# Optimization experiments

Measured on AMD Instinct MI355X. Metric: run time of the kernel, lower is better.

Reference implementation:

```python
import jax, jax.numpy as jnp
import numpy as np

N_NODES = 100000
N_EDGES = 1600000
NFEAT, NHID, NCLASS = 128, 64, 16


def setup_inputs() -> dict:
    key = jax.random.key(0)
    k1, k2, k3, k4, k5 = jax.random.split(key, 5)
    x = jax.random.normal(k1, (N_NODES, NFEAT), dtype=jnp.float32)
    edge_index = jax.random.randint(k2, (2, N_EDGES), 0, N_NODES, dtype=jnp.int64)
    edge_weight = jax.random.uniform(k3, (N_EDGES,), dtype=jnp.float32)
    # PyG Linear default init ~ kaiming-uniform; plain scaled normals suffice as a baseline
    W1 = jax.random.normal(k4, (NFEAT, NHID), dtype=jnp.float32) / np.sqrt(NFEAT)
    W2 = jax.random.normal(k5, (NHID, NCLASS), dtype=jnp.float32) / np.sqrt(NHID)
    return {"x": x, "edge_index": edge_index, "edge_weight": edge_weight, "W1": W1, "W2": W2}


def _gcn_conv(x, W, src, dst, w, num_nodes):
    # GCNConv(normalize=False, add_self_loops=False, bias=False):
    # out[dst] = sum_{e: dst(e)=dst} w_e * (x @ W)[src(e)]
    h = x @ W                                    # [N, out]
    msg = w[:, None] * h[src]                    # [E, out] gathered messages
    return jax.ops.segment_sum(msg, dst, num_segments=num_nodes)


def reference(x, edge_index, edge_weight, W1, W2):
    src, dst = edge_index[0], edge_index[1]
    h = jax.nn.relu(_gcn_conv(x, W1, src, dst, edge_weight, N_NODES))
    out = _gcn_conv(h, W2, src, dst, edge_weight, N_NODES)
    return out
```

## Files before the change

### kernel.cpp

```cpp
#include <hip/hip_runtime.h>

#define N_NODES 100000
#define N_EDGES 1600000
#define NFEAT 128
#define NHID 64
#define NCLASS 16

#define NPB 196
#define NB 511
#define HIST_EPT 16
#define HIST_BLOCKS ((N_EDGES + 256 * HIST_EPT - 1) / (256 * HIST_EPT))
#define FILL_EPT 8
#define FILL_BLOCKS ((N_EDGES + 256 * FILL_EPT - 1) / (256 * FILL_EPT))
#define NTILES ((N_NODES + 15) / 16)
#define GEMM_BLOCKS ((NTILES + 3) / 4)

typedef unsigned int u32;
typedef __attribute__((ext_vector_type(8))) short bf16x8;
typedef __attribute__((ext_vector_type(4))) float f32x4;

__device__ __forceinline__ u32 pack_bf16(float a, float b) {
    u32 ua = __float_as_uint(a);
    u32 ub = __float_as_uint(b);
    ua = (ua + 0x7fffu + ((ua >> 16) & 1u)) >> 16;
    ub = (ub + 0x7fffu + ((ub >> 16) & 1u)) >> 16;
    return ua | (ub << 16);
}
__device__ __forceinline__ short f2bf(float f) {
    u32 u = __float_as_uint(f);
    u = (u + 0x7fffu + ((u >> 16) & 1u)) >> 16;
    return (short)u;
}
__device__ __forceinline__ float bf16_lo(u32 u) { return __uint_as_float(u << 16); }
__device__ __forceinline__ float bf16_hi(u32 u) { return __uint_as_float(u & 0xffff0000u); }

__global__ void detect_kernel(const u32* __restrict__ ei, int* __restrict__ flag) {
    __shared__ int any_nz;
    if (threadIdx.x == 0) any_nz = 0;
    __syncthreads();
    u32 v = ei[2 * threadIdx.x + 1];
    if (v != 0) any_nz = 1;
    __syncthreads();
    if (threadIdx.x == 0) *flag = any_nz;
}

__device__ __forceinline__ int load_idx(const void* ei, int flag, size_t pos) {
    return flag ? ((const int*)ei)[pos] : (int)((const long long*)ei)[pos];
}

__global__ __launch_bounds__(256) void histA_kernel(const void* __restrict__ ei,
                                                    const int* __restrict__ flag,
                                                    int* __restrict__ ghist) {
    __shared__ int cnt[512];
    int t = threadIdx.x;
    cnt[t] = 0;
    cnt[t + 256] = 0;
    __syncthreads();
    int f = *flag;
    int base = blockIdx.x * 256 * HIST_EPT;
#pragma unroll
    for (int k = 0; k < HIST_EPT; ++k) {
        int e = base + k * 256 + t;
        if (e < N_EDGES) {
            int d = load_idx(ei, f, (size_t)N_EDGES + e);
            atomicAdd(&cnt[d / NPB], 1);
        }
    }
    __syncthreads();
    if (cnt[t] > 0) atomicAdd(&ghist[t], cnt[t]);
    if (cnt[t + 256] > 0) atomicAdd(&ghist[t + 256], cnt[t + 256]);
}

__global__ __launch_bounds__(512) void scanA_kernel(const int* __restrict__ ghist,
                                                    int* __restrict__ bstart,
                                                    int* __restrict__ gcursor) {
    __shared__ int lds[512];
    int t = threadIdx.x;
    int own = (t < NB) ? ghist[t] : 0;
    lds[t] = own;
    __syncthreads();
    for (int off = 1; off < 512; off <<= 1) {
        int v = (t >= off) ? lds[t - off] : 0;
        __syncthreads();
        lds[t] += v;
        __syncthreads();
    }
    int excl = lds[t] - own;
    bstart[t] = excl;
    if (t == 511) bstart[512] = lds[511];
    if (t < NB) gcursor[t] = excl;
}

__global__ __launch_bounds__(256) void fillA_kernel(const void* __restrict__ ei,
                                                    const int* __restrict__ flag,
                                                    const float* __restrict__ ew,
                                                    int* __restrict__ gcursor,
                                                    int2* __restrict__ ebuf) {
    __shared__ int cnt[512];
    __shared__ int base[512];
    int t = threadIdx.x;
    cnt[t] = 0;
    cnt[t + 256] = 0;
    __syncthreads();
    int f = *flag;
    int eb = blockIdx.x * 256 * FILL_EPT;
    int src[FILL_EPT], bin[FILL_EPT], rank[FILL_EPT];
    float w[FILL_EPT];
#pragma unroll
    for (int k = 0; k < FILL_EPT; ++k) {
        int e = eb + k * 256 + t;
        bin[k] = -1;
        if (e < N_EDGES) {
            int s = load_idx(ei, f, (size_t)e);
            int d = load_idx(ei, f, (size_t)N_EDGES + e);
            int b = d / NPB;
            src[k] = s | ((d - b * NPB) << 20);
            w[k] = ew[e];
            bin[k] = b;
            rank[k] = atomicAdd(&cnt[b], 1);
        }
    }
    __syncthreads();
    if (cnt[t] > 0) base[t] = atomicAdd(&gcursor[t], cnt[t]);
    if (cnt[t + 256] > 0) base[t + 256] = atomicAdd(&gcursor[t + 256], cnt[t + 256]);
    __syncthreads();
#pragma unroll
    for (int k = 0; k < FILL_EPT; ++k) {
        if (bin[k] >= 0) {
            int pos = base[bin[k]] + rank[k];
            ebuf[pos] = make_int2(src[k], __float_as_int(w[k]));
        }
    }
}

__global__ __launch_bounds__(256) void sortB_kernel(const int2* __restrict__ ebuf,
                                                    const int* __restrict__ bstart,
                                                    int2* __restrict__ ebuf2,
                                                    int* __restrict__ row_ptr) {
    __shared__ int cnt[NPB];
    __shared__ int sc[256];
    __shared__ int cur[NPB];
    int t = threadIdx.x, b = blockIdx.x;
    for (int i = t; i < NPB; i += 256) cnt[i] = 0;
    __syncthreads();
    int start = bstart[b], end = bstart[b + 1];
    for (int i = start + t; i < end; i += 256) {
        int dl = ((u32)ebuf[i].x) >> 20;
        atomicAdd(&cnt[dl], 1);
    }
    __syncthreads();
    int own = (t < NPB) ? cnt[t] : 0;
    sc[t] = own;
    __syncthreads();
    for (int off = 1; off < 256; off <<= 1) {
        int v = (t >= off) ? sc[t - off] : 0;
        __syncthreads();
        sc[t] += v;
        __syncthreads();
    }
    int excl = sc[t] - own;
    if (t < NPB) {
        cur[t] = excl;
        int node = b * NPB + t;
        if (node < N_NODES) row_ptr[node] = start + excl;
    }
    if (b == 0 && t == 0) row_ptr[N_NODES] = N_EDGES;
    __syncthreads();
    for (int i = start + t; i < end; i += 256) {
        int2 p = ebuf[i];
        int dl = ((u32)p.x) >> 20;
        int pos = start + atomicAdd(&cur[dl], 1);
        ebuf2[pos] = make_int2(p.x & 0xFFFFF, p.y);
    }
}

__global__ __launch_bounds__(256) void gemm1_kernel(const float* __restrict__ X,
                                                    const float* __restrict__ W,
                                                    u32* __restrict__ Y) {
    __shared__ float Wsh[NFEAT * NHID];
    int t = threadIdx.x;
    for (int i = t; i < NFEAT * NHID; i += 256) Wsh[i] = W[i];
    __syncthreads();
    int wid = t >> 6;
    int lane = t & 63;
    int r = lane & 15, g = lane >> 4;
    int m0 = (blockIdx.x * 4 + wid) * 16;
    if (m0 >= N_NODES) return;

    bf16x8 af[4][4];
#pragma unroll
    for (int nt = 0; nt < 4; ++nt)
#pragma unroll
        for (int kt = 0; kt < 4; ++kt)
#pragma unroll
            for (int j = 0; j < 8; ++j)
                af[nt][kt][j] = f2bf(Wsh[(kt * 32 + g * 8 + j) * NHID + nt * 16 + r]);

    const float* xr = X + (size_t)(m0 + r) * NFEAT + g * 8;
    bf16x8 bfr[4];
#pragma unroll
    for (int kt = 0; kt < 4; ++kt) {
        float4 v0 = *(const float4*)(xr + kt * 32);
        float4 v1 = *(const float4*)(xr + kt * 32 + 4);
        bfr[kt][0] = f2bf(v0.x); bfr[kt][1] = f2bf(v0.y);
        bfr[kt][2] = f2bf(v0.z); bfr[kt][3] = f2bf(v0.w);
        bfr[kt][4] = f2bf(v1.x); bfr[kt][5] = f2bf(v1.y);
        bfr[kt][6] = f2bf(v1.z); bfr[kt][7] = f2bf(v1.w);
    }

    u32* yr = Y + (size_t)(m0 + r) * (NHID / 2);
#pragma unroll
    for (int nt = 0; nt < 4; ++nt) {
        f32x4 acc = {0.f, 0.f, 0.f, 0.f};
#pragma unroll
        for (int kt = 0; kt < 4; ++kt)
            acc = __builtin_amdgcn_mfma_f32_16x16x32_bf16(af[nt][kt], bfr[kt], acc, 0, 0, 0);
        uint2 o;
        o.x = pack_bf16(acc[0], acc[1]);
        o.y = pack_bf16(acc[2], acc[3]);
        *(uint2*)(yr + nt * 8 + g * 2) = o;
    }
}

__global__ __launch_bounds__(256) void gemm2_kernel(const u32* __restrict__ Hb,
                                                    const float* __restrict__ W,
                                                    u32* __restrict__ Y) {
    __shared__ float Wsh[NHID * NCLASS];
    int t = threadIdx.x;
    for (int i = t; i < NHID * NCLASS; i += 256) Wsh[i] = W[i];
    __syncthreads();
    int wid = t >> 6;
    int lane = t & 63;
    int r = lane & 15, g = lane >> 4;
    int m0 = (blockIdx.x * 4 + wid) * 16;
    if (m0 >= N_NODES) return;

    bf16x8 af[2];
#pragma unroll
    for (int kt = 0; kt < 2; ++kt)
#pragma unroll
        for (int j = 0; j < 8; ++j)
            af[kt][j] = f2bf(Wsh[(kt * 32 + g * 8 + j) * NCLASS + r]);

    const u32* hr = Hb + (size_t)(m0 + r) * (NHID / 2) + g * 4;
    bf16x8 b0 = *(const bf16x8*)(hr + 0);
    bf16x8 b1 = *(const bf16x8*)(hr + 16);

    f32x4 acc = {0.f, 0.f, 0.f, 0.f};
    acc = __builtin_amdgcn_mfma_f32_16x16x32_bf16(af[0], b0, acc, 0, 0, 0);
    acc = __builtin_amdgcn_mfma_f32_16x16x32_bf16(af[1], b1, acc, 0, 0, 0);

    u32* yr = Y + (size_t)(m0 + r) * (NCLASS / 2);
    uint2 o;
    o.x = pack_bf16(acc[0], acc[1]);
    o.y = pack_bf16(acc[2], acc[3]);
    *(uint2*)(yr + g * 2) = o;
}

__global__ __launch_bounds__(256) void agg1_kernel(const u32* __restrict__ xwb,
                                                   const int* __restrict__ row_ptr,
                                                   const int2* __restrict__ ep,
                                                   u32* __restrict__ hb) {
    int t = blockIdx.x * 256 + threadIdx.x;
    int node = t >> 6;
    int lane = t & 63;
    int p = lane & 15;
    int sub = lane >> 4;
    if (node >= N_NODES) return;
    int start = row_ptr[node], end = row_ptr[node + 1];
    float f0 = 0.f, f1 = 0.f, f2 = 0.f, f3 = 0.f;
    float g0 = 0.f, g1 = 0.f, g2 = 0.f, g3 = 0.f;
    int i = start + sub;
    for (; i + 4 < end; i += 8) {
        int2 pa = ep[i];
        int2 pb = ep[i + 4];
        uint2 ua = *(const uint2*)(xwb + (size_t)pa.x * 32 + 2 * p);
        uint2 ub = *(const uint2*)(xwb + (size_t)pb.x * 32 + 2 * p);
        float wa = __int_as_float(pa.y);
        float wb = __int_as_float(pb.y);
        f0 += wa * bf16_lo(ua.x); f1 += wa * bf16_hi(ua.x);
        f2 += wa * bf16_lo(ua.y); f3 += wa * bf16_hi(ua.y);
        g0 += wb * bf16_lo(ub.x); g1 += wb * bf16_hi(ub.x);
        g2 += wb * bf16_lo(ub.y); g3 += wb * bf16_hi(ub.y);
    }
    if (i < end) {
        int2 pa = ep[i];
        uint2 ua = *(const uint2*)(xwb + (size_t)pa.x * 32 + 2 * p);
        float wa = __int_as_float(pa.y);
        f0 += wa * bf16_lo(ua.x); f1 += wa * bf16_hi(ua.x);
        f2 += wa * bf16_lo(ua.y); f3 += wa * bf16_hi(ua.y);
    }
    f0 += g0; f1 += g1; f2 += g2; f3 += g3;
    f0 += __shfl_xor(f0, 16, 64); f1 += __shfl_xor(f1, 16, 64);
    f2 += __shfl_xor(f2, 16, 64); f3 += __shfl_xor(f3, 16, 64);
    f0 += __shfl_xor(f0, 32, 64); f1 += __shfl_xor(f1, 32, 64);
    f2 += __shfl_xor(f2, 32, 64); f3 += __shfl_xor(f3, 32, 64);
    if (sub == 0) {
        uint2 o;
        o.x = pack_bf16(fmaxf(f0, 0.f), fmaxf(f1, 0.f));
        o.y = pack_bf16(fmaxf(f2, 0.f), fmaxf(f3, 0.f));
        *(uint2*)(hb + (size_t)node * 32 + 2 * p) = o;
    }
}

__global__ __launch_bounds__(256) void agg2_kernel(const u32* __restrict__ hwb,
                                                   const int* __restrict__ row_ptr,
                                                   const int2* __restrict__ ep,
                                                   float* __restrict__ out) {
    int t = blockIdx.x * 256 + threadIdx.x;
    int node = t >> 6;
    int lane = t & 63;
    int p = lane & 3;
    int sub = lane >> 2;
    if (node >= N_NODES) return;
    int start = row_ptr[node], end = row_ptr[node + 1];
    float f0 = 0.f, f1 = 0.f, f2 = 0.f, f3 = 0.f;
    for (int i = start + sub; i < end; i += 16) {
        int2 pr = ep[i];
        uint2 u = *(const uint2*)(hwb + (size_t)pr.x * 8 + 2 * p);
        float w = __int_as_float(pr.y);
        f0 += w * bf16_lo(u.x); f1 += w * bf16_hi(u.x);
        f2 += w * bf16_lo(u.y); f3 += w * bf16_hi(u.y);
    }
    f0 += __shfl_xor(f0, 4, 64);  f1 += __shfl_xor(f1, 4, 64);
    f2 += __shfl_xor(f2, 4, 64);  f3 += __shfl_xor(f3, 4, 64);
    f0 += __shfl_xor(f0, 8, 64);  f1 += __shfl_xor(f1, 8, 64);
    f2 += __shfl_xor(f2, 8, 64);  f3 += __shfl_xor(f3, 8, 64);
    f0 += __shfl_xor(f0, 16, 64); f1 += __shfl_xor(f1, 16, 64);
    f2 += __shfl_xor(f2, 16, 64); f3 += __shfl_xor(f3, 16, 64);
    f0 += __shfl_xor(f0, 32, 64); f1 += __shfl_xor(f1, 32, 64);
    f2 += __shfl_xor(f2, 32, 64); f3 += __shfl_xor(f3, 32, 64);
    if (sub == 0) {
        *(float4*)(out + (size_t)node * NCLASS + 4 * p) = make_float4(f0, f1, f2, f3);
    }
}

extern "C" void kernel_launch(void* const* d_in, const int* in_sizes, int n_in,
                              void* d_out, int out_size, void* d_ws, size_t ws_size,
                              hipStream_t stream) {
    const float* x  = (const float*)d_in[0];
    const void*  ei = d_in[1];
    const float* ew = (const float*)d_in[2];
    const float* W1 = (const float*)d_in[3];
    const float* W2 = (const float*)d_in[4];
    float* out = (float*)d_out;

    char* ws = (char*)d_ws;
    size_t off = 0;
    auto take = [&](size_t bytes) {
        char* p = ws + off;
        off += (bytes + 511) & ~(size_t)511;
        return p;
    };
    int*   flag    = (int*)take(4);
    int*   ghist   = (int*)take(512 * 4);
    int*   bstart  = (int*)take(513 * 4);
    int*   gcursor = (int*)take(512 * 4);
    int*   row_ptr = (int*)take((size_t)(N_NODES + 1) * 4);
    int2*  ebuf    = (int2*)take((size_t)N_EDGES * 8);
    int2*  ebuf2   = (int2*)take((size_t)N_EDGES * 8);
    u32*   xwb     = (u32*)take((size_t)N_NODES * (NHID / 2) * 4);
    u32*   hb      = (u32*)take((size_t)N_NODES * (NHID / 2) * 4);
    u32*   hwb     = xwb;

    detect_kernel<<<1, 256, 0, stream>>>((const u32*)ei, flag);
    hipMemsetAsync(ghist, 0, 512 * 4, stream);
    histA_kernel<<<HIST_BLOCKS, 256, 0, stream>>>(ei, flag, ghist);
    scanA_kernel<<<1, 512, 0, stream>>>(ghist, bstart, gcursor);
    fillA_kernel<<<FILL_BLOCKS, 256, 0, stream>>>(ei, flag, ew, gcursor, ebuf);
    sortB_kernel<<<NB, 256, 0, stream>>>(ebuf, bstart, ebuf2, row_ptr);

    gemm1_kernel<<<GEMM_BLOCKS, 256, 0, stream>>>(x, W1, xwb);
    agg1_kernel<<<(N_NODES * 64 + 255) / 256, 256, 0, stream>>>(xwb, row_ptr, ebuf2, hb);
    gemm2_kernel<<<GEMM_BLOCKS, 256, 0, stream>>>(hb, W2, hwb);
    agg2_kernel<<<(N_NODES * 64 + 255) / 256, 256, 0, stream>>>(hwb, row_ptr, ebuf2, out);
}
```

Before: 168.7 us.

## Fuse GEMM1 with histogram, fold GEMM2 into aggregation, inline index-width detection

The first GEMM and the destination histogram now run in one launch, with blocks split by index range, so the two independent stages overlap. The layer-2 GEMM moves into the first aggregation kernel: each wave applies ReLU and multiplies by a transposed W2 held in LDS. That removes the hidden-activation round trip through memory and two launches. The separate detect kernel is replaced by a per-wave ballot over the index array inside the hist and fill kernels. The cost is more shuffles and LDS reads per node in the aggregation, plus redundant detection loads in every block.

```diff
diff --git a/kernel.cpp b/kernel.cpp
--- a/kernel.cpp
+++ b/kernel.cpp
@@ -34,41 +34,84 @@
 __device__ __forceinline__ float bf16_lo(u32 u) { return __uint_as_float(u << 16); }
 __device__ __forceinline__ float bf16_hi(u32 u) { return __uint_as_float(u & 0xffff0000u); }
 
-__global__ void detect_kernel(const u32* __restrict__ ei, int* __restrict__ flag) {
-    __shared__ int any_nz;
-    if (threadIdx.x == 0) any_nz = 0;
-    __syncthreads();
-    u32 v = ei[2 * threadIdx.x + 1];
-    if (v != 0) any_nz = 1;
-    __syncthreads();
-    if (threadIdx.x == 0) *flag = any_nz;
+__device__ __forceinline__ int detect_i32(const void* ei) {
+    u32 v = ((const u32*)ei)[2 * (threadIdx.x & 63) + 1];
+    return (__ballot(v != 0) != 0ULL) ? 1 : 0;
 }
 
 __device__ __forceinline__ int load_idx(const void* ei, int flag, size_t pos) {
     return flag ? ((const int*)ei)[pos] : (int)((const long long*)ei)[pos];
 }
 
-__global__ __launch_bounds__(256) void histA_kernel(const void* __restrict__ ei,
-                                                    const int* __restrict__ flag,
+__global__ __launch_bounds__(256) void mega1_kernel(const float* __restrict__ X,
+                                                    const float* __restrict__ W,
+                                                    u32* __restrict__ Y,
+                                                    const void* __restrict__ ei,
                                                     int* __restrict__ ghist) {
-    __shared__ int cnt[512];
+    __shared__ float Wsh[NFEAT * NHID];
     int t = threadIdx.x;
-    cnt[t] = 0;
-    cnt[t + 256] = 0;
-    __syncthreads();
-    int f = *flag;
-    int base = blockIdx.x * 256 * HIST_EPT;
-#pragma unroll
-    for (int k = 0; k < HIST_EPT; ++k) {
-        int e = base + k * 256 + t;
-        if (e < N_EDGES) {
-            int d = load_idx(ei, f, (size_t)N_EDGES + e);
-            atomicAdd(&cnt[d / NPB], 1);
-        }
-    }
-    __syncthreads();
-    if (cnt[t] > 0) atomicAdd(&ghist[t], cnt[t]);
-    if (cnt[t + 256] > 0) atomicAdd(&ghist[t + 256], cnt[t + 256]);
+    if (blockIdx.x < GEMM_BLOCKS) {
+        for (int i = t; i < NFEAT * NHID; i += 256) Wsh[i] = W[i];
+        __syncthreads();
+        int wid = t >> 6;
+        int lane = t & 63;
+        int r = lane & 15, g = lane >> 4;
+        int m0 = (blockIdx.x * 4 + wid) * 16;
+        if (m0 >= N_NODES) return;
+
+        bf16x8 af[4][4];
+#pragma unroll
+        for (int nt = 0; nt < 4; ++nt)
+#pragma unroll
+            for (int kt = 0; kt < 4; ++kt)
+#pragma unroll
+                for (int j = 0; j < 8; ++j)
+                    af[nt][kt][j] = f2bf(Wsh[(kt * 32 + g * 8 + j) * NHID + nt * 16 + r]);
+
+        const float* xr = X + (size_t)(m0 + r) * NFEAT + g * 8;
+        bf16x8 bfr[4];
+#pragma unroll
+        for (int kt = 0; kt < 4; ++kt) {
+            float4 v0 = *(const float4*)(xr + kt * 32);
+            float4 v1 = *(const float4*)(xr + kt * 32 + 4);
+            bfr[kt][0] = f2bf(v0.x); bfr[kt][1] = f2bf(v0.y);
+            bfr[kt][2] = f2bf(v0.z); bfr[kt][3] = f2bf(v0.w);
+            bfr[kt][4] = f2bf(v1.x); bfr[kt][5] = f2bf(v1.y);
+            bfr[kt][6] = f2bf(v1.z); bfr[kt][7] = f2bf(v1.w);
+        }
+
+        u32* yr = Y + (size_t)(m0 + r) * (NHID / 2);
+#pragma unroll
+        for (int nt = 0; nt < 4; ++nt) {
+            f32x4 acc = {0.f, 0.f, 0.f, 0.f};
+#pragma unroll
+            for (int kt = 0; kt < 4; ++kt)
+                acc = __builtin_amdgcn_mfma_f32_16x16x32_bf16(af[nt][kt], bfr[kt], acc, 0, 0, 0);
+            uint2 o;
+            o.x = pack_bf16(acc[0], acc[1]);
+            o.y = pack_bf16(acc[2], acc[3]);
+            *(uint2*)(yr + nt * 8 + g * 2) = o;
+        }
+    } else {
+        int* cnt = (int*)Wsh;
+        int bid = blockIdx.x - GEMM_BLOCKS;
+        cnt[t] = 0;
+        cnt[t + 256] = 0;
+        __syncthreads();
+        int f = detect_i32(ei);
+        int base = bid * 256 * HIST_EPT;
+#pragma unroll
+        for (int k = 0; k < HIST_EPT; ++k) {
+            int e = base + k * 256 + t;
+            if (e < N_EDGES) {
+                int d = load_idx(ei, f, (size_t)N_EDGES + e);
+                atomicAdd(&cnt[d / NPB], 1);
+            }
+        }
+        __syncthreads();
+        if (cnt[t] > 0) atomicAdd(&ghist[t], cnt[t]);
+        if (cnt[t + 256] > 0) atomicAdd(&ghist[t + 256], cnt[t + 256]);
+    }
 }
 
 __global__ __launch_bounds__(512) void scanA_kernel(const int* __restrict__ ghist,
@@ -92,7 +135,6 @@
 }
 
 __global__ __launch_bounds__(256) void fillA_kernel(const void* __restrict__ ei,
-                                                    const int* __restrict__ flag,
                                                     const float* __restrict__ ew,
                                                     int* __restrict__ gcursor,
                                                     int2* __restrict__ ebuf) {
@@ -102,7 +144,7 @@
     cnt[t] = 0;
     cnt[t + 256] = 0;
     __syncthreads();
-    int f = *flag;
+    int f = detect_i32(ei);
     int eb = blockIdx.x * 256 * FILL_EPT;
     int src[FILL_EPT], bin[FILL_EPT], rank[FILL_EPT];
     float w[FILL_EPT];
@@ -174,133 +216,80 @@
     }
 }
 
-__global__ __launch_bounds__(256) void gemm1_kernel(const float* __restrict__ X,
-                                                    const float* __restrict__ W,
-                                                    u32* __restrict__ Y) {
-    __shared__ float Wsh[NFEAT * NHID];
-    int t = threadIdx.x;
-    for (int i = t; i < NFEAT * NHID; i += 256) Wsh[i] = W[i];
-    __syncthreads();
-    int wid = t >> 6;
-    int lane = t & 63;
-    int r = lane & 15, g = lane >> 4;
-    int m0 = (blockIdx.x * 4 + wid) * 16;
-    if (m0 >= N_NODES) return;
-
-    bf16x8 af[4][4];
-#pragma unroll
-    for (int nt = 0; nt < 4; ++nt)
-#pragma unroll
-        for (int kt = 0; kt < 4; ++kt)
-#pragma unroll
-            for (int j = 0; j < 8; ++j)
-                af[nt][kt][j] = f2bf(Wsh[(kt * 32 + g * 8 + j) * NHID + nt * 16 + r]);
-
-    const float* xr = X + (size_t)(m0 + r) * NFEAT + g * 8;
-    bf16x8 bfr[4];
-#pragma unroll
-    for (int kt = 0; kt < 4; ++kt) {
-        float4 v0 = *(const float4*)(xr + kt * 32);
-        float4 v1 = *(const float4*)(xr + kt * 32 + 4);
-        bfr[kt][0] = f2bf(v0.x); bfr[kt][1] = f2bf(v0.y);
-        bfr[kt][2] = f2bf(v0.z); bfr[kt][3] = f2bf(v0.w);
-        bfr[kt][4] = f2bf(v1.x); bfr[kt][5] = f2bf(v1.y);
-        bfr[kt][6] = f2bf(v1.z); bfr[kt][7] = f2bf(v1.w);
-    }
-
-    u32* yr = Y + (size_t)(m0 + r) * (NHID / 2);
-#pragma unroll
-    for (int nt = 0; nt < 4; ++nt) {
-        f32x4 acc = {0.f, 0.f, 0.f, 0.f};
-#pragma unroll
-        for (int kt = 0; kt < 4; ++kt)
-            acc = __builtin_amdgcn_mfma_f32_16x16x32_bf16(af[nt][kt], bfr[kt], acc, 0, 0, 0);
-        uint2 o;
-        o.x = pack_bf16(acc[0], acc[1]);
-        o.y = pack_bf16(acc[2], acc[3]);
-        *(uint2*)(yr + nt * 8 + g * 2) = o;
-    }
-}
-
-__global__ __launch_bounds__(256) void gemm2_kernel(const u32* __restrict__ Hb,
-                                                    const float* __restrict__ W,
-                                                    u32* __restrict__ Y) {
-    __shared__ float Wsh[NHID * NCLASS];
-    int t = threadIdx.x;
-    for (int i = t; i < NHID * NCLASS; i += 256) Wsh[i] = W[i];
-    __syncthreads();
-    int wid = t >> 6;
-    int lane = t & 63;
-    int r = lane & 15, g = lane >> 4;
-    int m0 = (blockIdx.x * 4 + wid) * 16;
-    if (m0 >= N_NODES) return;
-
-    bf16x8 af[2];
-#pragma unroll
-    for (int kt = 0; kt < 2; ++kt)
-#pragma unroll
-        for (int j = 0; j < 8; ++j)
-            af[kt][j] = f2bf(Wsh[(kt * 32 + g * 8 + j) * NCLASS + r]);
-
-    const u32* hr = Hb + (size_t)(m0 + r) * (NHID / 2) + g * 4;
-    bf16x8 b0 = *(const bf16x8*)(hr + 0);
-    bf16x8 b1 = *(const bf16x8*)(hr + 16);
-
-    f32x4 acc = {0.f, 0.f, 0.f, 0.f};
-    acc = __builtin_amdgcn_mfma_f32_16x16x32_bf16(af[0], b0, acc, 0, 0, 0);
-    acc = __builtin_amdgcn_mfma_f32_16x16x32_bf16(af[1], b1, acc, 0, 0, 0);
-
-    u32* yr = Y + (size_t)(m0 + r) * (NCLASS / 2);
-    uint2 o;
-    o.x = pack_bf16(acc[0], acc[1]);
-    o.y = pack_bf16(acc[2], acc[3]);
-    *(uint2*)(yr + g * 2) = o;
-}
-
-__global__ __launch_bounds__(256) void agg1_kernel(const u32* __restrict__ xwb,
-                                                   const int* __restrict__ row_ptr,
-                                                   const int2* __restrict__ ep,
-                                                   u32* __restrict__ hb) {
-    int t = blockIdx.x * 256 + threadIdx.x;
+__global__ __launch_bounds__(256) void agg1f_kernel(const u32* __restrict__ xwb,
+                                                    const int* __restrict__ row_ptr,
+                                                    const int2* __restrict__ ep,
+                                                    const float* __restrict__ W2,
+                                                    u32* __restrict__ hwb) {
+    __shared__ float W2t[NCLASS * NHID];
+    int tt = threadIdx.x;
+    for (int i = tt; i < NCLASS * NHID; i += 256) {
+        int c = i >> 6, k = i & 63;
+        W2t[i] = W2[k * NCLASS + c];
+    }
+    __syncthreads();
+    int t = blockIdx.x * 256 + tt;
     int node = t >> 6;
     int lane = t & 63;
-    int p = lane & 15;
-    int sub = lane >> 4;
+    int p = lane & 7;
+    int sub = lane >> 3;
     if (node >= N_NODES) return;
     int start = row_ptr[node], end = row_ptr[node + 1];
     float f0 = 0.f, f1 = 0.f, f2 = 0.f, f3 = 0.f;
+    float f4 = 0.f, f5 = 0.f, f6 = 0.f, f7 = 0.f;
     float g0 = 0.f, g1 = 0.f, g2 = 0.f, g3 = 0.f;
+    float g4 = 0.f, g5 = 0.f, g6 = 0.f, g7 = 0.f;
     int i = start + sub;
-    for (; i + 4 < end; i += 8) {
+    for (; i + 8 < end; i += 16) {
         int2 pa = ep[i];
-        int2 pb = ep[i + 4];
-        uint2 ua = *(const uint2*)(xwb + (size_t)pa.x * 32 + 2 * p);
-        uint2 ub = *(const uint2*)(xwb + (size_t)pb.x * 32 + 2 * p);
+        int2 pb = ep[i + 8];
+        uint4 ua = *(const uint4*)(xwb + (size_t)pa.x * 32 + 4 * p);
+        uint4 ub = *(const uint4*)(xwb + (size_t)pb.x * 32 + 4 * p);
         float wa = __int_as_float(pa.y);
         float wb = __int_as_float(pb.y);
         f0 += wa * bf16_lo(ua.x); f1 += wa * bf16_hi(ua.x);
         f2 += wa * bf16_lo(ua.y); f3 += wa * bf16_hi(ua.y);
+        f4 += wa * bf16_lo(ua.z); f5 += wa * bf16_hi(ua.z);
+        f6 += wa * bf16_lo(ua.w); f7 += wa * bf16_hi(ua.w);
         g0 += wb * bf16_lo(ub.x); g1 += wb * bf16_hi(ub.x);
         g2 += wb * bf16_lo(ub.y); g3 += wb * bf16_hi(ub.y);
+        g4 += wb * bf16_lo(ub.z); g5 += wb * bf16_hi(ub.z);
+        g6 += wb * bf16_lo(ub.w); g7 += wb * bf16_hi(ub.w);
     }
     if (i < end) {
         int2 pa = ep[i];
-        uint2 ua = *(const uint2*)(xwb + (size_t)pa.x * 32 + 2 * p);
+        uint4 ua = *(const uint4*)(xwb + (size_t)pa.x * 32 + 4 * p);
         float wa = __int_as_float(pa.y);
         f0 += wa * bf16_lo(ua.x); f1 += wa * bf16_hi(ua.x);
         f2 += wa * bf16_lo(ua.y); f3 += wa * bf16_hi(ua.y);
+        f4 += wa * bf16_lo(ua.z); f5 += wa * bf16_hi(ua.z);
+        f6 += wa * bf16_lo(ua.w); f7 += wa * bf16_hi(ua.w);
     }
     f0 += g0; f1 += g1; f2 += g2; f3 += g3;
-    f0 += __shfl_xor(f0, 16, 64); f1 += __shfl_xor(f1, 16, 64);
-    f2 += __shfl_xor(f2, 16, 64); f3 += __shfl_xor(f3, 16, 64);
-    f0 += __shfl_xor(f0, 32, 64); f1 += __shfl_xor(f1, 32, 64);
-    f2 += __shfl_xor(f2, 32, 64); f3 += __shfl_xor(f3, 32, 64);
-    if (sub == 0) {
-        uint2 o;
-        o.x = pack_bf16(fmaxf(f0, 0.f), fmaxf(f1, 0.f));
-        o.y = pack_bf16(fmaxf(f2, 0.f), fmaxf(f3, 0.f));
-        *(uint2*)(hb + (size_t)node * 32 + 2 * p) = o;
-    }
+    f4 += g4; f5 += g5; f6 += g6; f7 += g7;
+#pragma unroll
+    for (int m = 8; m <= 32; m <<= 1) {
+        f0 += __shfl_xor(f0, m, 64); f1 += __shfl_xor(f1, m, 64);
+        f2 += __shfl_xor(f2, m, 64); f3 += __shfl_xor(f3, m, 64);
+        f4 += __shfl_xor(f4, m, 64); f5 += __shfl_xor(f5, m, 64);
+        f6 += __shfl_xor(f6, m, 64); f7 += __shfl_xor(f7, m, 64);
+    }
+    f0 = fmaxf(f0, 0.f); f1 = fmaxf(f1, 0.f);
+    f2 = fmaxf(f2, 0.f); f3 = fmaxf(f3, 0.f);
+    f4 = fmaxf(f4, 0.f); f5 = fmaxf(f5, 0.f);
+    f6 = fmaxf(f6, 0.f); f7 = fmaxf(f7, 0.f);
+    const float* w0 = &W2t[(2 * sub) * NHID + 8 * p];
+    const float* w1 = &W2t[(2 * sub + 1) * NHID + 8 * p];
+    float po0 = f0 * w0[0] + f1 * w0[1] + f2 * w0[2] + f3 * w0[3]
+              + f4 * w0[4] + f5 * w0[5] + f6 * w0[6] + f7 * w0[7];
+    float po1 = f0 * w1[0] + f1 * w1[1] + f2 * w1[2] + f3 * w1[3]
+              + f4 * w1[4] + f5 * w1[5] + f6 * w1[6] + f7 * w1[7];
+#pragma unroll
+    for (int m = 1; m <= 4; m <<= 1) {
+        po0 += __shfl_xor(po0, m, 64);
+        po1 += __shfl_xor(po1, m, 64);
+    }
+    if (p == 0) hwb[(size_t)node * 8 + sub] = pack_bf16(po0, po1);
 }
 
 __global__ __launch_bounds__(256) void agg2_kernel(const u32* __restrict__ hwb,
@@ -322,14 +311,11 @@
         f0 += w * bf16_lo(u.x); f1 += w * bf16_hi(u.x);
         f2 += w * bf16_lo(u.y); f3 += w * bf16_hi(u.y);
     }
-    f0 += __shfl_xor(f0, 4, 64);  f1 += __shfl_xor(f1, 4, 64);
-    f2 += __shfl_xor(f2, 4, 64);  f3 += __shfl_xor(f3, 4, 64);
-    f0 += __shfl_xor(f0, 8, 64);  f1 += __shfl_xor(f1, 8, 64);
-    f2 += __shfl_xor(f2, 8, 64);  f3 += __shfl_xor(f3, 8, 64);
-    f0 += __shfl_xor(f0, 16, 64); f1 += __shfl_xor(f1, 16, 64);
-    f2 += __shfl_xor(f2, 16, 64); f3 += __shfl_xor(f3, 16, 64);
-    f0 += __shfl_xor(f0, 32, 64); f1 += __shfl_xor(f1, 32, 64);
-    f2 += __shfl_xor(f2, 32, 64); f3 += __shfl_xor(f3, 32, 64);
+#pragma unroll
+    for (int m = 4; m <= 32; m <<= 1) {
+        f0 += __shfl_xor(f0, m, 64); f1 += __shfl_xor(f1, m, 64);
+        f2 += __shfl_xor(f2, m, 64); f3 += __shfl_xor(f3, m, 64);
+    }
     if (sub == 0) {
         *(float4*)(out + (size_t)node * NCLASS + 4 * p) = make_float4(f0, f1, f2, f3);
     }
@@ -352,7 +338,6 @@
         off += (bytes + 511) & ~(size_t)511;
         return p;
     };
-    int*   flag    = (int*)take(4);
     int*   ghist   = (int*)take(512 * 4);
     int*   bstart  = (int*)take(513 * 4);
     int*   gcursor = (int*)take(512 * 4);
@@ -360,18 +345,14 @@
     int2*  ebuf    = (int2*)take((size_t)N_EDGES * 8);
     int2*  ebuf2   = (int2*)take((size_t)N_EDGES * 8);
     u32*   xwb     = (u32*)take((size_t)N_NODES * (NHID / 2) * 4);
-    u32*   hb      = (u32*)take((size_t)N_NODES * (NHID / 2) * 4);
-    u32*   hwb     = xwb;
-
-    detect_kernel<<<1, 256, 0, stream>>>((const u32*)ei, flag);
+    u32*   hwb     = (u32*)take((size_t)N_NODES * (NCLASS / 2) * 4);
+
     hipMemsetAsync(ghist, 0, 512 * 4, stream);
-    histA_kernel<<<HIST_BLOCKS, 256, 0, stream>>>(ei, flag, ghist);
+    mega1_kernel<<<GEMM_BLOCKS + HIST_BLOCKS, 256, 0, stream>>>(x, W1, xwb, ei, ghist);
     scanA_kernel<<<1, 512, 0, stream>>>(ghist, bstart, gcursor);
-    fillA_kernel<<<FILL_BLOCKS, 256, 0, stream>>>(ei, flag, ew, gcursor, ebuf);
+    fillA_kernel<<<FILL_BLOCKS, 256, 0, stream>>>(ei, ew, gcursor, ebuf);
     sortB_kernel<<<NB, 256, 0, stream>>>(ebuf, bstart, ebuf2, row_ptr);
 
-    gemm1_kernel<<<GEMM_BLOCKS, 256, 0, stream>>>(x, W1, xwb);
-    agg1_kernel<<<(N_NODES * 64 + 255) / 256, 256, 0, stream>>>(xwb, row_ptr, ebuf2, hb);
-    gemm2_kernel<<<GEMM_BLOCKS, 256, 0, stream>>>(hb, W2, hwb);
+    agg1f_kernel<<<(N_NODES * 64 + 255) / 256, 256, 0, stream>>>(xwb, row_ptr, ebuf2, W2, hwb);
     agg2_kernel<<<(N_NODES * 64 + 255) / 256, 256, 0, stream>>>(hwb, row_ptr, ebuf2, out);
 }
```

After: 192.7 us. 1.14x slower.

## Switch to fp16 storage and half2 accumulation; fuse gemm1 with histogram; inline index detect

Applied to the files above, without the earlier changes.

Changes intermediate storage and MFMA inputs from bf16 to fp16, and accumulates the edge aggregations in packed half2 FMAs instead of fp32 scalar FMAs. Merges the first GEMM and the destination histogram into one launch by splitting blocks between the two roles. Replaces the separate index-width detect kernel with a per-wavefront ballot, which removes two launches. Accumulating sums of about 16 weighted terms in fp16 raises rounding error and adds some overflow risk.

```diff
diff --git a/kernel.cpp b/kernel.cpp
--- a/kernel.cpp
+++ b/kernel.cpp
@@ -1,4 +1,5 @@
 #include <hip/hip_runtime.h>
+#include <hip/hip_fp16.h>
 
 #define N_NODES 100000
 #define N_EDGES 1600000
@@ -16,59 +17,91 @@
 #define GEMM_BLOCKS ((NTILES + 3) / 4)
 
 typedef unsigned int u32;
-typedef __attribute__((ext_vector_type(8))) short bf16x8;
+typedef __attribute__((ext_vector_type(8))) _Float16 f16x8;
 typedef __attribute__((ext_vector_type(4))) float f32x4;
 
-__device__ __forceinline__ u32 pack_bf16(float a, float b) {
-    u32 ua = __float_as_uint(a);
-    u32 ub = __float_as_uint(b);
-    ua = (ua + 0x7fffu + ((ua >> 16) & 1u)) >> 16;
-    ub = (ub + 0x7fffu + ((ub >> 16) & 1u)) >> 16;
-    return ua | (ub << 16);
-}
-__device__ __forceinline__ short f2bf(float f) {
-    u32 u = __float_as_uint(f);
-    u = (u + 0x7fffu + ((u >> 16) & 1u)) >> 16;
-    return (short)u;
-}
-__device__ __forceinline__ float bf16_lo(u32 u) { return __uint_as_float(u << 16); }
-__device__ __forceinline__ float bf16_hi(u32 u) { return __uint_as_float(u & 0xffff0000u); }
-
-__global__ void detect_kernel(const u32* __restrict__ ei, int* __restrict__ flag) {
-    __shared__ int any_nz;
-    if (threadIdx.x == 0) any_nz = 0;
-    __syncthreads();
-    u32 v = ei[2 * threadIdx.x + 1];
-    if (v != 0) any_nz = 1;
-    __syncthreads();
-    if (threadIdx.x == 0) *flag = any_nz;
+__device__ __forceinline__ __half2 u2h2(u32 u) { __half2 h; __builtin_memcpy(&h, &u, 4); return h; }
+__device__ __forceinline__ u32 h22u(__half2 h) { u32 u; __builtin_memcpy(&u, &h, 4); return u; }
+__device__ __forceinline__ u32 pack_h16(float a, float b) { return h22u(__floats2half2_rn(a, b)); }
+
+__device__ __forceinline__ int detect_i32(const void* ei) {
+    u32 v = ((const u32*)ei)[2 * (threadIdx.x & 63) + 1];
+    return (__ballot(v != 0) != 0ULL) ? 1 : 0;
 }
 
 __device__ __forceinline__ int load_idx(const void* ei, int flag, size_t pos) {
     return flag ? ((const int*)ei)[pos] : (int)((const long long*)ei)[pos];
 }
 
-__global__ __launch_bounds__(256) void histA_kernel(const void* __restrict__ ei,
-                                                    const int* __restrict__ flag,
+__global__ __launch_bounds__(256) void mega1_kernel(const float* __restrict__ X,
+                                                    const float* __restrict__ W,
+                                                    u32* __restrict__ Y,
+                                                    const void* __restrict__ ei,
                                                     int* __restrict__ ghist) {
-    __shared__ int cnt[512];
+    __shared__ float Wsh[NFEAT * NHID];
     int t = threadIdx.x;
-    cnt[t] = 0;
-    cnt[t + 256] = 0;
-    __syncthreads();
-    int f = *flag;
-    int base = blockIdx.x * 256 * HIST_EPT;
-#pragma unroll
-    for (int k = 0; k < HIST_EPT; ++k) {
-        int e = base + k * 256 + t;
-        if (e < N_EDGES) {
-            int d = load_idx(ei, f, (size_t)N_EDGES + e);
-            atomicAdd(&cnt[d / NPB], 1);
-        }
-    }
-    __syncthreads();
-    if (cnt[t] > 0) atomicAdd(&ghist[t], cnt[t]);
-    if (cnt[t + 256] > 0) atomicAdd(&ghist[t + 256], cnt[t + 256]);
+    if (blockIdx.x < GEMM_BLOCKS) {
+        for (int i = t; i < NFEAT * NHID; i += 256) Wsh[i] = W[i];
+        __syncthreads();
+        int wid = t >> 6;
+        int lane = t & 63;
+        int r = lane & 15, g = lane >> 4;
+        int m0 = (blockIdx.x * 4 + wid) * 16;
+        if (m0 >= N_NODES) return;
+
+        f16x8 af[4][4];
+#pragma unroll
+        for (int nt = 0; nt < 4; ++nt)
+#pragma unroll
+            for (int kt = 0; kt < 4; ++kt)
+#pragma unroll
+                for (int j = 0; j < 8; ++j)
+                    af[nt][kt][j] = (_Float16)Wsh[(kt * 32 + g * 8 + j) * NHID + nt * 16 + r];
+
+        const float* xr = X + (size_t)(m0 + r) * NFEAT + g * 8;
+        f16x8 bfr[4];
+#pragma unroll
+        for (int kt = 0; kt < 4; ++kt) {
+            float4 v0 = *(const float4*)(xr + kt * 32);
+            float4 v1 = *(const float4*)(xr + kt * 32 + 4);
+            bfr[kt][0] = (_Float16)v0.x; bfr[kt][1] = (_Float16)v0.y;
+            bfr[kt][2] = (_Float16)v0.z; bfr[kt][3] = (_Float16)v0.w;
+            bfr[kt][4] = (_Float16)v1.x; bfr[kt][5] = (_Float16)v1.y;
+            bfr[kt][6] = (_Float16)v1.z; bfr[kt][7] = (_Float16)v1.w;
+        }
+
+        u32* yr = Y + (size_t)(m0 + r) * (NHID / 2);
+#pragma unroll
+        for (int nt = 0; nt < 4; ++nt) {
+            f32x4 acc = {0.f, 0.f, 0.f, 0.f};
+#pragma unroll
+            for (int kt = 0; kt < 4; ++kt)
+                acc = __builtin_amdgcn_mfma_f32_16x16x32_f16(af[nt][kt], bfr[kt], acc, 0, 0, 0);
+            uint2 o;
+            o.x = pack_h16(acc[0], acc[1]);
+            o.y = pack_h16(acc[2], acc[3]);
+            *(uint2*)(yr + nt * 8 + g * 2) = o;
+        }
+    } else {
+        int* cnt = (int*)Wsh;
+        int bid = blockIdx.x - GEMM_BLOCKS;
+        cnt[t] = 0;
+        cnt[t + 256] = 0;
+        __syncthreads();
+        int f = detect_i32(ei);
+        int base = bid * 256 * HIST_EPT;
+#pragma unroll
+        for (int k = 0; k < HIST_EPT; ++k) {
+            int e = base + k * 256 + t;
+            if (e < N_EDGES) {
+                int d = load_idx(ei, f, (size_t)N_EDGES + e);
+                atomicAdd(&cnt[d / NPB], 1);
+            }
+        }
+        __syncthreads();
+        if (cnt[t] > 0) atomicAdd(&ghist[t], cnt[t]);
+        if (cnt[t + 256] > 0) atomicAdd(&ghist[t + 256], cnt[t + 256]);
+    }
 }
 
 __global__ __launch_bounds__(512) void scanA_kernel(const int* __restrict__ ghist,
@@ -92,7 +125,6 @@
 }
 
 __global__ __launch_bounds__(256) void fillA_kernel(const void* __restrict__ ei,
-                                                    const int* __restrict__ flag,
                                                     const float* __restrict__ ew,
                                                     int* __restrict__ gcursor,
                                                     int2* __restrict__ ebuf) {
@@ -102,7 +134,7 @@
     cnt[t] = 0;
     cnt[t + 256] = 0;
     __syncthreads();
-    int f = *flag;
+    int f = detect_i32(ei);
     int eb = blockIdx.x * 256 * FILL_EPT;
     int src[FILL_EPT], bin[FILL_EPT], rank[FILL_EPT];
     float w[FILL_EPT];
@@ -174,54 +206,6 @@
     }
 }
 
-__global__ __launch_bounds__(256) void gemm1_kernel(const float* __restrict__ X,
-                                                    const float* __restrict__ W,
-                                                    u32* __restrict__ Y) {
-    __shared__ float Wsh[NFEAT * NHID];
-    int t = threadIdx.x;
-    for (int i = t; i < NFEAT * NHID; i += 256) Wsh[i] = W[i];
-    __syncthreads();
-    int wid = t >> 6;
-    int lane = t & 63;
-    int r = lane & 15, g = lane >> 4;
-    int m0 = (blockIdx.x * 4 + wid) * 16;
-    if (m0 >= N_NODES) return;
-
-    bf16x8 af[4][4];
-#pragma unroll
-    for (int nt = 0; nt < 4; ++nt)
-#pragma unroll
-        for (int kt = 0; kt < 4; ++kt)
-#pragma unroll
-            for (int j = 0; j < 8; ++j)
-                af[nt][kt][j] = f2bf(Wsh[(kt * 32 + g * 8 + j) * NHID + nt * 16 + r]);
-
-    const float* xr = X + (size_t)(m0 + r) * NFEAT + g * 8;
-    bf16x8 bfr[4];
-#pragma unroll
-    for (int kt = 0; kt < 4; ++kt) {
-        float4 v0 = *(const float4*)(xr + kt * 32);
-        float4 v1 = *(const float4*)(xr + kt * 32 + 4);
-        bfr[kt][0] = f2bf(v0.x); bfr[kt][1] = f2bf(v0.y);
-        bfr[kt][2] = f2bf(v0.z); bfr[kt][3] = f2bf(v0.w);
-        bfr[kt][4] = f2bf(v1.x); bfr[kt][5] = f2bf(v1.y);
-        bfr[kt][6] = f2bf(v1.z); bfr[kt][7] = f2bf(v1.w);
-    }
-
-    u32* yr = Y + (size_t)(m0 + r) * (NHID / 2);
-#pragma unroll
-    for (int nt = 0; nt < 4; ++nt) {
-        f32x4 acc = {0.f, 0.f, 0.f, 0.f};
-#pragma unroll
-        for (int kt = 0; kt < 4; ++kt)
-            acc = __builtin_amdgcn_mfma_f32_16x16x32_bf16(af[nt][kt], bfr[kt], acc, 0, 0, 0);
-        uint2 o;
-        o.x = pack_bf16(acc[0], acc[1]);
-        o.y = pack_bf16(acc[2], acc[3]);
-        *(uint2*)(yr + nt * 8 + g * 2) = o;
-    }
-}
-
 __global__ __launch_bounds__(256) void gemm2_kernel(const u32* __restrict__ Hb,
                                                     const float* __restrict__ W,
                                                     u32* __restrict__ Y) {
@@ -235,25 +219,26 @@
     int m0 = (blockIdx.x * 4 + wid) * 16;
     if (m0 >= N_NODES) return;
 
-    bf16x8 af[2];
+    f16x8 af[2];
 #pragma unroll
     for (int kt = 0; kt < 2; ++kt)
 #pragma unroll
         for (int j = 0; j < 8; ++j)
-            af[kt][j] = f2bf(Wsh[(kt * 32 + g * 8 + j) * NCLASS + r]);
+            af[kt][j] = (_Float16)Wsh[(kt * 32 + g * 8 + j) * NCLASS + r];
 
     const u32* hr = Hb + (size_t)(m0 + r) * (NHID / 2) + g * 4;
-    bf16x8 b0 = *(const bf16x8*)(hr + 0);
-    bf16x8 b1 = *(const bf16x8*)(hr + 16);
+    union { uint4 u; f16x8 h; } b0, b1;
+    b0.u = *(const uint4*)(hr + 0);
+    b1.u = *(const uint4*)(hr + 16);
 
     f32x4 acc = {0.f, 0.f, 0.f, 0.f};
-    acc = __builtin_amdgcn_mfma_f32_16x16x32_bf16(af[0], b0, acc, 0, 0, 0);
-    acc = __builtin_amdgcn_mfma_f32_16x16x32_bf16(af[1], b1, acc, 0, 0, 0);
+    acc = __builtin_amdgcn_mfma_f32_16x16x32_f16(af[0], b0.h, acc, 0, 0, 0);
+    acc = __builtin_amdgcn_mfma_f32_16x16x32_f16(af[1], b1.h, acc, 0, 0, 0);
 
     u32* yr = Y + (size_t)(m0 + r) * (NCLASS / 2);
     uint2 o;
-    o.x = pack_bf16(acc[0], acc[1]);
-    o.y = pack_bf16(acc[2], acc[3]);
+    o.x = pack_h16(acc[0], acc[1]);
+    o.y = pack_h16(acc[2], acc[3]);
     *(uint2*)(yr + g * 2) = o;
 }
 
@@ -268,37 +253,40 @@
     int sub = lane >> 4;
     if (node >= N_NODES) return;
     int start = row_ptr[node], end = row_ptr[node + 1];
-    float f0 = 0.f, f1 = 0.f, f2 = 0.f, f3 = 0.f;
-    float g0 = 0.f, g1 = 0.f, g2 = 0.f, g3 = 0.f;
+    __half2 a0 = u2h2(0), a1 = u2h2(0), b0 = u2h2(0), b1 = u2h2(0);
     int i = start + sub;
     for (; i + 4 < end; i += 8) {
         int2 pa = ep[i];
         int2 pb = ep[i + 4];
         uint2 ua = *(const uint2*)(xwb + (size_t)pa.x * 32 + 2 * p);
         uint2 ub = *(const uint2*)(xwb + (size_t)pb.x * 32 + 2 * p);
-        float wa = __int_as_float(pa.y);
-        float wb = __int_as_float(pb.y);
-        f0 += wa * bf16_lo(ua.x); f1 += wa * bf16_hi(ua.x);
-        f2 += wa * bf16_lo(ua.y); f3 += wa * bf16_hi(ua.y);
-        g0 += wb * bf16_lo(ub.x); g1 += wb * bf16_hi(ub.x);
-        g2 += wb * bf16_lo(ub.y); g3 += wb * bf16_hi(ub.y);
+        __half2 wa = __half2half2(__float2half(__int_as_float(pa.y)));
+        __half2 wb = __half2half2(__float2half(__int_as_float(pb.y)));
+        a0 = __hfma2(u2h2(ua.x), wa, a0);
+        a1 = __hfma2(u2h2(ua.y), wa, a1);
+        b0 = __hfma2(u2h2(ub.x), wb, b0);
+        b1 = __hfma2(u2h2(ub.y), wb, b1);
     }
     if (i < end) {
         int2 pa = ep[i];
         uint2 ua = *(const uint2*)(xwb + (size_t)pa.x * 32 + 2 * p);
-        float wa = __int_as_float(pa.y);
-        f0 += wa * bf16_lo(ua.x); f1 += wa * bf16_hi(ua.x);
-        f2 += wa * bf16_lo(ua.y); f3 += wa * bf16_hi(ua.y);
-    }
-    f0 += g0; f1 += g1; f2 += g2; f3 += g3;
-    f0 += __shfl_xor(f0, 16, 64); f1 += __shfl_xor(f1, 16, 64);
-    f2 += __shfl_xor(f2, 16, 64); f3 += __shfl_xor(f3, 16, 64);
-    f0 += __shfl_xor(f0, 32, 64); f1 += __shfl_xor(f1, 32, 64);
-    f2 += __shfl_xor(f2, 32, 64); f3 += __shfl_xor(f3, 32, 64);
+        __half2 wa = __half2half2(__float2half(__int_as_float(pa.y)));
+        a0 = __hfma2(u2h2(ua.x), wa, a0);
+        a1 = __hfma2(u2h2(ua.y), wa, a1);
+    }
+    a0 = __hadd2(a0, b0);
+    a1 = __hadd2(a1, b1);
+#pragma unroll
+    for (int m = 16; m <= 32; m <<= 1) {
+        a0 = __hadd2(a0, u2h2((u32)__shfl_xor((int)h22u(a0), m, 64)));
+        a1 = __hadd2(a1, u2h2((u32)__shfl_xor((int)h22u(a1), m, 64)));
+    }
     if (sub == 0) {
+        float2 f0 = __half22float2(a0);
+        float2 f1 = __half22float2(a1);
         uint2 o;
-        o.x = pack_bf16(fmaxf(f0, 0.f), fmaxf(f1, 0.f));
-        o.y = pack_bf16(fmaxf(f2, 0.f), fmaxf(f3, 0.f));
+        o.x = pack_h16(fmaxf(f0.x, 0.f), fmaxf(f0.y, 0.f));
+        o.y = pack_h16(fmaxf(f1.x, 0.f), fmaxf(f1.y, 0.f));
         *(uint2*)(hb + (size_t)node * 32 + 2 * p) = o;
     }
 }
@@ -314,24 +302,24 @@
     int sub = lane >> 2;
     if (node >= N_NODES) return;
     int start = row_ptr[node], end = row_ptr[node + 1];
-    float f0 = 0.f, f1 = 0.f, f2 = 0.f, f3 = 0.f;
+    __half2 a0 = u2h2(0), a1 = u2h2(0);
     for (int i = start + sub; i < end; i += 16) {
         int2 pr = ep[i];
         uint2 u = *(const uint2*)(hwb + (size_t)pr.x * 8 + 2 * p);
-        float w = __int_as_float(pr.y);
-        f0 += w * bf16_lo(u.x); f1 += w * bf16_hi(u.x);
-        f2 += w * bf16_lo(u.y); f3 += w * bf16_hi(u.y);
-    }
-    f0 += __shfl_xor(f0, 4, 64);  f1 += __shfl_xor(f1, 4, 64);
-    f2 += __shfl_xor(f2, 4, 64);  f3 += __shfl_xor(f3, 4, 64);
-    f0 += __shfl_xor(f0, 8, 64);  f1 += __shfl_xor(f1, 8, 64);
-    f2 += __shfl_xor(f2, 8, 64);  f3 += __shfl_xor(f3, 8, 64);
-    f0 += __shfl_xor(f0, 16, 64); f1 += __shfl_xor(f1, 16, 64);
-    f2 += __shfl_xor(f2, 16, 64); f3 += __shfl_xor(f3, 16, 64);
-    f0 += __shfl_xor(f0, 32, 64); f1 += __shfl_xor(f1, 32, 64);
-    f2 += __shfl_xor(f2, 32, 64); f3 += __shfl_xor(f3, 32, 64);
+        __half2 w2 = __half2half2(__float2half(__int_as_float(pr.y)));
+        a0 = __hfma2(u2h2(u.x), w2, a0);
+        a1 = __hfma2(u2h2(u.y), w2, a1);
+    }
+#pragma unroll
+    for (int m = 4; m <= 32; m <<= 1) {
+        a0 = __hadd2(a0, u2h2((u32)__shfl_xor((int)h22u(a0), m, 64)));
+        a1 = __hadd2(a1, u2h2((u32)__shfl_xor((int)h22u(a1), m, 64)));
+    }
     if (sub == 0) {
-        *(float4*)(out + (size_t)node * NCLASS + 4 * p) = make_float4(f0, f1, f2, f3);
+        float2 f0 = __half22float2(a0);
+        float2 f1 = __half22float2(a1);
+        *(float4*)(out + (size_t)node * NCLASS + 4 * p) =
+            make_float4(f0.x, f0.y, f1.x, f1.y);
     }
 }
 
@@ -352,7 +340,6 @@
         off += (bytes + 511) & ~(size_t)511;
         return p;
     };
-    int*   flag    = (int*)take(4);
     int*   ghist   = (int*)take(512 * 4);
     int*   bstart  = (int*)take(513 * 4);
     int*   gcursor = (int*)take(512 * 4);
@@ -361,16 +348,14 @@
     int2*  ebuf2   = (int2*)take((size_t)N_EDGES * 8);
     u32*   xwb     = (u32*)take((size_t)N_NODES * (NHID / 2) * 4);
     u32*   hb      = (u32*)take((size_t)N_NODES * (NHID / 2) * 4);
-    u32*   hwb     = xwb;
-
-    detect_kernel<<<1, 256, 0, stream>>>((const u32*)ei, flag);
+    u32*   hwb     = (u32*)take((size_t)N_NODES * (NCLASS / 2) * 4);
+
     hipMemsetAsync(ghist, 0, 512 * 4, stream);
-    histA_kernel<<<HIST_BLOCKS, 256, 0, stream>>>(ei, flag, ghist);
+    mega1_kernel<<<GEMM_BLOCKS + HIST_BLOCKS, 256, 0, stream>>>(x, W1, xwb, ei, ghist);
     scanA_kernel<<<1, 512, 0, stream>>>(ghist, bstart, gcursor);
-    fillA_kernel<<<FILL_BLOCKS, 256, 0, stream>>>(ei, flag, ew, gcursor, ebuf);
+    fillA_kernel<<<FILL_BLOCKS, 256, 0, stream>>>(ei, ew, gcursor, ebuf);
     sortB_kernel<<<NB, 256, 0, stream>>>(ebuf, bstart, ebuf2, row_ptr);
 
-    gemm1_kernel<<<GEMM_BLOCKS, 256, 0, stream>>>(x, W1, xwb);
     agg1_kernel<<<(N_NODES * 64 + 255) / 256, 256, 0, stream>>>(xwb, row_ptr, ebuf2, hb);
     gemm2_kernel<<<GEMM_BLOCKS, 256, 0, stream>>>(hb, W2, hwb);
     agg2_kernel<<<(N_NODES * 64 + 255) / 256, 256, 0, stream>>>(hwb, row_ptr, ebuf2, out);
```

After: 159.7 us. 1.06x faster.
